# Performance work log

Hardware: AMD Instinct MI355X
Metric: run time of the kernel (lower is better)

Reference implementation:

```python
import jax, jax.numpy as jnp
import numpy as np


def setup_inputs() -> dict:
    key = jax.random.key(0)
    k1, k2, k3, k4 = jax.random.split(key, 4)
    B, S, IN, H = 4, 2048, 512, 1024
    x = jax.random.normal(k1, (B, S, IN), dtype=jnp.float32)
    W1 = jax.random.normal(k2, (IN, H), dtype=jnp.float32) * (1.0 / np.sqrt(IN))
    b1 = jax.random.normal(k3, (H,), dtype=jnp.float32) * 0.02
    Wq = jax.random.normal(k4, (H, H), dtype=jnp.float32) * (1.0 / np.sqrt(H))
    return {"x": x, "W1": W1, "b1": b1, "Wq": Wq, "atten_size": 16}


def reference(x, W1, b1, Wq, atten_size):
    A = atten_size
    B, S, _ = x.shape
    H = W1.shape[1]
    h = jax.nn.relu(jnp.einsum('bsi,ih->bsh', x, W1) + b1)  # [B,S,H]
    # zero-pad sequence dim by A on each side
    padded = jnp.pad(h, ((0, 0), (A, A), (0, 0)))  # [B,S+2A,H]
    # torch: stack(roll(padded, k, 1) for k in -A..A, dim=2) then slice [A:-A]
    # => x_nei[b, i, j] = padded[b, 2A + i - j]
    idx = 2 * A + jnp.arange(S)[:, None] - jnp.arange(2 * A + 1)[None, :]  # [S,W]
    x_nei = padded[:, idx, :]  # [B,S,W,H]
    q = jnp.einsum('bsh,hk->bsk', h, Wq)  # [B,S,H]
    scores = jnp.einsum('bsh,bswh->bsw', q, x_nei) / jnp.sqrt(jnp.asarray(H, x.dtype))
    w = jax.nn.softmax(scores, axis=2)  # softmax over window axis
    out = jnp.einsum('bsw,bswh->bsh', w, x_nei)
    return out
```

## Files before the change

kernel.cpp:

```cpp
#include <hip/hip_runtime.h>
#include <stdint.h>

constexpr int BATCH = 4;
constexpr int SEQ   = 2048;
constexpr int DIN   = 512;
constexpr int DH    = 1024;
constexpr int BS    = BATCH * SEQ;
constexpr int AP    = 32;
constexpr int AW    = 64;

typedef float  floatx4 __attribute__((ext_vector_type(4)));
typedef short  bf16x8  __attribute__((ext_vector_type(8)));

static __device__ __forceinline__ unsigned short f2bf(float f) {
  union { float f; unsigned u; } v; v.f = f;
  unsigned r = (v.u + 0x7fffu + ((v.u >> 16) & 1u)) >> 16;
  return (unsigned short)r;
}

__global__ __launch_bounds__(256) void to_bf16_k(const float* __restrict__ in,
                                                 unsigned short* __restrict__ out, int n) {
  int i = (blockIdx.x * 256 + threadIdx.x) * 4;
  if (i < n) {
    float4 v = *(const float4*)(in + i);
    ushort4 o;
    o.x = f2bf(v.x); o.y = f2bf(v.y); o.z = f2bf(v.z); o.w = f2bf(v.w);
    *(ushort4*)(out + i) = o;
  }
}

__global__ __launch_bounds__(256) void transpose_bf16_k(const float* __restrict__ in,
                                                        unsigned short* __restrict__ out,
                                                        int R, int C) {
  __shared__ float t[32][33];
  int c0 = blockIdx.x * 32, r0 = blockIdx.y * 32;
  int tx = threadIdx.x & 31, ty = threadIdx.x >> 5;
  for (int i = ty; i < 32; i += 8) t[i][tx] = in[(size_t)(r0 + i) * C + c0 + tx];
  __syncthreads();
  for (int i = ty; i < 32; i += 8) out[(size_t)(c0 + i) * R + r0 + tx] = f2bf(t[tx][i]);
}

template <bool RELU>
__global__ __launch_bounds__(256) void gemm_bt(const unsigned short* __restrict__ Ab,
                                               const unsigned short* __restrict__ Bt,
                                               const float* __restrict__ bias,
                                               unsigned short* __restrict__ outB,
                                               unsigned short* __restrict__ outBT,
                                               int M, int N, int K) {
  __shared__ __align__(16) short As[128 * 32];
  __shared__ __align__(16) short Bs[128 * 32];
  const int tid  = threadIdx.x;
  const int m0   = blockIdx.y * 128, n0 = blockIdx.x * 128;
  const int wave = tid >> 6, lane = tid & 63;
  const int wm   = (wave >> 1) * 64, wn = (wave & 1) * 64;
  const int l16  = lane & 15, quad = lane >> 4;

  const int sr = tid >> 1;
  const int sh = (tid & 1) * 16;
  const uint4* gA = (const uint4*)(Ab + (size_t)(m0 + sr) * K + sh);
  const uint4* gB = (const uint4*)(Bt + (size_t)(n0 + sr) * K + sh);
  uint4* lA = (uint4*)&As[sr * 32 + sh];
  uint4* lB = (uint4*)&Bs[sr * 32 + sh];

  floatx4 acc[4][4];
  for (int i = 0; i < 4; i++)
    for (int j = 0; j < 4; j++) acc[i][j] = {0.f, 0.f, 0.f, 0.f};

  const int ksteps = K >> 5;
  for (int ks = 0; ks < ksteps; ++ks) {
    uint4 a0 = gA[0], a1 = gA[1];
    uint4 b0 = gB[0], b1 = gB[1];
    gA += 4; gB += 4;
    __syncthreads();
    lA[0] = a0; lA[1] = a1;
    lB[0] = b0; lB[1] = b1;
    __syncthreads();
    bf16x8 af[4], bfr[4];
    for (int i = 0; i < 4; i++)
      af[i] = *(const bf16x8*)&As[(wm + i * 16 + l16) * 32 + quad * 8];
    for (int j = 0; j < 4; j++)
      bfr[j] = *(const bf16x8*)&Bs[(wn + j * 16 + l16) * 32 + quad * 8];
    for (int i = 0; i < 4; i++)
      for (int j = 0; j < 4; j++)
        acc[i][j] = __builtin_amdgcn_mfma_f32_16x16x32_bf16(af[i], bfr[j], acc[i][j], 0, 0, 0);
  }

  for (int j = 0; j < 4; j++) {
    const int col = n0 + wn + j * 16 + l16;
    const float bv = RELU ? bias[col] : 0.f;
    for (int i = 0; i < 4; i++) {
      const int rowb = m0 + wm + i * 16 + quad * 4;
      float v[4];
      for (int r = 0; r < 4; r++) {
        v[r] = acc[i][j][r] + bv;
        if (RELU) v[r] = fmaxf(v[r], 0.f);
      }
      if (outB) {
        for (int r = 0; r < 4; r++) outB[(size_t)(rowb + r) * N + col] = f2bf(v[r]);
      }
      if (outBT) {
        ushort4 o4; o4.x = f2bf(v[0]); o4.y = f2bf(v[1]); o4.z = f2bf(v[2]); o4.w = f2bf(v[3]);
        *(ushort4*)(outBT + (size_t)col * M + rowb) = o4;
      }
    }
  }
}

__global__ __launch_bounds__(512) void attn_mfma_k(const unsigned short* __restrict__ hb,
                                                   const unsigned short* __restrict__ hbT,
                                                   const unsigned short* __restrict__ qb,
                                                   float* __restrict__ out) {
  __shared__ __align__(16) short Qs[32 * 72];
  __shared__ __align__(16) short Hs[64 * 72];
  __shared__ __align__(16) short Ps[32 * 72];
  __shared__ __align__(16) short Ht[128 * 72];
  __shared__ float Sf[32 * 64];

  const int tid  = threadIdx.x;
  const int wave = tid >> 6, lane = tid & 63;
  const int l16  = lane & 15, quad = lane >> 4;
  const int p0   = blockIdx.x * AP;
  const int s0   = p0 & (SEQ - 1);

  for (int i = tid; i < 32 * 72 / 2; i += 512) ((unsigned*)Ps)[i] = 0;

  const int mtile = wave >> 2;
  const int ntile = wave & 3;
  const bool isQ = tid < 128;
  const bool isH = (tid >= 128) && (tid < 384);
  const int sq = tid & 3;
  int srow = isQ ? (tid >> 2) : ((tid - 128) >> 2);
  bool ldv = false;
  const uint4* gsrc = nullptr;
  short* ldst = nullptr;
  if (isQ) {
    ldv = true;
    gsrc = (const uint4*)(qb + (size_t)(p0 + srow) * DH + sq * 16);
    ldst = &Qs[srow * 72 + sq * 16];
  } else if (isH) {
    const int hj = s0 - 16 + srow;
    ldv = (hj >= 0) && (hj < SEQ);
    gsrc = (const uint4*)(hb + (long long)(p0 - 16 + srow) * DH + sq * 16);
    ldst = &Hs[srow * 72 + sq * 16];
  }

  floatx4 acc = {0.f, 0.f, 0.f, 0.f};
  for (int ks = 0; ks < DH / 64; ++ks) {
    uint4 r0 = {0, 0, 0, 0}, r1 = {0, 0, 0, 0};
    if (ldv) { r0 = gsrc[0]; r1 = gsrc[1]; gsrc += 8; }
    __syncthreads();
    if (isQ || isH) { ((uint4*)ldst)[0] = r0; ((uint4*)ldst)[1] = r1; }
    __syncthreads();
    bf16x8 a0 = *(const bf16x8*)&Qs[(mtile * 16 + l16) * 72 + quad * 8];
    bf16x8 a1 = *(const bf16x8*)&Qs[(mtile * 16 + l16) * 72 + 32 + quad * 8];
    bf16x8 b0 = *(const bf16x8*)&Hs[(ntile * 16 + l16) * 72 + quad * 8];
    bf16x8 b1 = *(const bf16x8*)&Hs[(ntile * 16 + l16) * 72 + 32 + quad * 8];
    acc = __builtin_amdgcn_mfma_f32_16x16x32_bf16(a0, b0, acc, 0, 0, 0);
    acc = __builtin_amdgcn_mfma_f32_16x16x32_bf16(a1, b1, acc, 0, 0, 0);
  }
  for (int r = 0; r < 4; r++)
    Sf[(mtile * 16 + quad * 4 + r) * 64 + ntile * 16 + l16] = acc[r] * (1.f / 32.f);
  __syncthreads();

  {
    const int row = tid >> 4, k = tid & 15;
    const float v0 = Sf[row * 64 + row + k];
    const float v1 = Sf[row * 64 + row + k + 16];
    const float v2 = (k == 0) ? Sf[row * 64 + row + 32] : -1e30f;
    float mx = fmaxf(v0, fmaxf(v1, v2));
    for (int off = 1; off < 16; off <<= 1) mx = fmaxf(mx, __shfl_xor(mx, off, 64));
    const float e0 = __expf(v0 - mx), e1 = __expf(v1 - mx);
    const float e2 = (k == 0) ? __expf(v2 - mx) : 0.f;
    float sum = e0 + e1 + e2;
    for (int off = 1; off < 16; off <<= 1) sum += __shfl_xor(sum, off, 64);
    const float inv = 1.f / sum;
    Ps[row * 72 + row + k] = f2bf(e0 * inv);
    Ps[row * 72 + row + k + 16] = f2bf(e1 * inv);
    if (k == 0) Ps[row * 72 + row + 32] = f2bf(e2 * inv);
  }
  __syncthreads();

  const bf16x8 pa0 = *(const bf16x8*)&Ps[(mtile * 16 + l16) * 72 + quad * 8];
  const bf16x8 pa1 = *(const bf16x8*)&Ps[(mtile * 16 + l16) * 72 + 32 + quad * 8];

  int lo = 16 - s0; if (lo < 0) lo = 0;
  int hi = SEQ + 16 - s0; if (hi > AW) hi = AW;
  const bool interior = (lo == 0) && (hi == AW);
  const int hn = tid >> 2;
  const int ntp = (wave & 3) * 2;

  for (int c = 0; c < DH / 128; ++c) {
    const int nc = c * 128;
    const unsigned short* hp = hbT + ((long long)(nc + hn) * BS + p0 - 16 + sq * 16);
    uint4 r0 = ((const uint4*)hp)[0], r1 = ((const uint4*)hp)[1];
    if (!interior) {
      unsigned short vals[16];
      ((uint4*)vals)[0] = r0; ((uint4*)vals)[1] = r1;
      #pragma unroll
      for (int e = 0; e < 16; e++) {
        const int k = sq * 16 + e;
        if (k < lo || k >= hi) vals[e] = 0;
      }
      r0 = ((uint4*)vals)[0]; r1 = ((uint4*)vals)[1];
    }
    __syncthreads();
    ((uint4*)&Ht[hn * 72 + sq * 16])[0] = r0;
    ((uint4*)&Ht[hn * 72 + sq * 16])[1] = r1;
    __syncthreads();
    floatx4 acc2[2] = {{0.f, 0.f, 0.f, 0.f}, {0.f, 0.f, 0.f, 0.f}};
    for (int t = 0; t < 2; t++) {
      const int nt = ntp + t;
      bf16x8 b0 = *(const bf16x8*)&Ht[(nt * 16 + l16) * 72 + quad * 8];
      bf16x8 b1 = *(const bf16x8*)&Ht[(nt * 16 + l16) * 72 + 32 + quad * 8];
      acc2[t] = __builtin_amdgcn_mfma_f32_16x16x32_bf16(pa0, b0, acc2[t], 0, 0, 0);
      acc2[t] = __builtin_amdgcn_mfma_f32_16x16x32_bf16(pa1, b1, acc2[t], 0, 0, 0);
    }
    for (int t = 0; t < 2; t++) {
      const int col = nc + (ntp + t) * 16 + l16;
      for (int r = 0; r < 4; r++)
        out[(size_t)(p0 + mtile * 16 + quad * 4 + r) * DH + col] = acc2[t][r];
    }
  }
}

extern "C" void kernel_launch(void* const* d_in, const int* in_sizes, int n_in,
                              void* d_out, int out_size, void* d_ws, size_t ws_size,
                              hipStream_t stream) {
  const float* x  = (const float*)d_in[0];
  const float* W1 = (const float*)d_in[1];
  const float* b1 = (const float*)d_in[2];
  const float* Wq = (const float*)d_in[3];

  char* w = (char*)d_ws;
  unsigned short* xb  = (unsigned short*)(w);
  unsigned short* w1t = (unsigned short*)(w + (8ull  << 20));
  unsigned short* wqt = (unsigned short*)(w + (9ull  << 20));
  unsigned short* hb  = (unsigned short*)(w + (11ull << 20));
  unsigned short* hbT = (unsigned short*)(w + (27ull << 20));
  unsigned short* qb  = (unsigned short*)(w + (43ull << 20));

  to_bf16_k<<<(BS * DIN) / (256 * 4), 256, 0, stream>>>(x, xb, BS * DIN);
  transpose_bf16_k<<<dim3(DH / 32, DIN / 32), 256, 0, stream>>>(W1, w1t, DIN, DH);
  transpose_bf16_k<<<dim3(DH / 32, DH / 32), 256, 0, stream>>>(Wq, wqt, DH, DH);

  gemm_bt<true><<<dim3(DH / 128, BS / 128), 256, 0, stream>>>(xb, w1t, b1, hb, hbT, BS, DH, DIN);
  gemm_bt<false><<<dim3(DH / 128, BS / 128), 256, 0, stream>>>(hb, wqt, nullptr, qb, nullptr, BS, DH, DH);

  attn_mfma_k<<<BS / AP, 512, 0, stream>>>(hb, hbT, qb, (float*)d_out);
}
```

Before: 172.2 us.

## Use direct global-to-LDS loads in GEMM and split hT transpose into own kernel

The GEMM tile loads now use global_load_lds to write straight from global memory into shared memory, instead of staging through registers. The LDS layout becomes a per-wave contiguous arrangement. The strided transposed store of h from the first GEMM epilogue moves into a separate tiled transpose kernel that reads the bf16 h back. This aims to cut register pressure and the uncoalesced epilogue writes, at the cost of an extra launch and an extra read and write pass over h.

```diff
diff --git a/kernel.cpp b/kernel.cpp
--- a/kernel.cpp
+++ b/kernel.cpp
@@ -16,6 +16,12 @@
   union { float f; unsigned u; } v; v.f = f;
   unsigned r = (v.u + 0x7fffu + ((v.u >> 16) & 1u)) >> 16;
   return (unsigned short)r;
+}
+
+static __device__ __forceinline__ void gld_lds16(const unsigned short* g, const short* l) {
+  typedef const __attribute__((address_space(1))) void* gvp;
+  typedef __attribute__((address_space(3))) void* lvp;
+  __builtin_amdgcn_global_load_lds((gvp)(uintptr_t)g, (lvp)(unsigned)(uintptr_t)l, 16, 0, 0);
 }
 
 __global__ __launch_bounds__(256) void to_bf16_k(const float* __restrict__ in,
@@ -40,27 +46,50 @@
   for (int i = ty; i < 32; i += 8) out[(size_t)(c0 + i) * R + r0 + tx] = f2bf(t[tx][i]);
 }
 
+__global__ __launch_bounds__(256) void transpose_hb_k(const unsigned short* __restrict__ in,
+                                                      unsigned short* __restrict__ out) {
+  __shared__ __align__(16) unsigned short t[64][80];
+  const int tid = threadIdx.x;
+  const int r0 = blockIdx.x * 64;
+  const int c0 = blockIdx.y * 64;
+  const int tr = tid >> 2, tc = (tid & 3) * 16;
+  const uint4* src = (const uint4*)(in + (size_t)(r0 + tr) * DH + c0 + tc);
+  uint4 v0 = src[0], v1 = src[1];
+  *(uint4*)&t[tr][tc]     = v0;
+  *(uint4*)&t[tr][tc + 8] = v1;
+  __syncthreads();
+  __align__(16) unsigned short vals[16];
+  #pragma unroll
+  for (int e = 0; e < 16; e++) vals[e] = t[tc + e][tr];
+  uint4* dst = (uint4*)(out + (size_t)(c0 + tr) * BS + r0 + tc);
+  dst[0] = ((uint4*)vals)[0];
+  dst[1] = ((uint4*)vals)[1];
+}
+
 template <bool RELU>
 __global__ __launch_bounds__(256) void gemm_bt(const unsigned short* __restrict__ Ab,
                                                const unsigned short* __restrict__ Bt,
                                                const float* __restrict__ bias,
                                                unsigned short* __restrict__ outB,
-                                               unsigned short* __restrict__ outBT,
                                                int M, int N, int K) {
   __shared__ __align__(16) short As[128 * 32];
   __shared__ __align__(16) short Bs[128 * 32];
   const int tid  = threadIdx.x;
   const int m0   = blockIdx.y * 128, n0 = blockIdx.x * 128;
-  const int wave = tid >> 6, lane = tid & 63;
-  const int wm   = (wave >> 1) * 64, wn = (wave & 1) * 64;
+  const int wv   = tid >> 6, lane = tid & 63;
+  const int wm   = (wv >> 1) * 64, wn = (wv & 1) * 64;
   const int l16  = lane & 15, quad = lane >> 4;
 
-  const int sr = tid >> 1;
-  const int sh = (tid & 1) * 16;
-  const uint4* gA = (const uint4*)(Ab + (size_t)(m0 + sr) * K + sh);
-  const uint4* gB = (const uint4*)(Bt + (size_t)(n0 + sr) * K + sh);
-  uint4* lA = (uint4*)&As[sr * 32 + sh];
-  uint4* lB = (uint4*)&Bs[sr * 32 + sh];
+  const int ra = lane >> 2;
+  const int ca = (lane & 3) * 8;
+  const unsigned short* gA0 = Ab + (size_t)(m0 + wv * 32 + ra) * K + ca;
+  const unsigned short* gA1 = Ab + (size_t)(m0 + wv * 32 + 16 + ra) * K + ca;
+  const unsigned short* gB0 = Bt + (size_t)(n0 + wv * 32 + ra) * K + ca;
+  const unsigned short* gB1 = Bt + (size_t)(n0 + wv * 32 + 16 + ra) * K + ca;
+  const short* lA0 = &As[wv * 1024];
+  const short* lA1 = &As[wv * 1024 + 512];
+  const short* lB0 = &Bs[wv * 1024];
+  const short* lB1 = &Bs[wv * 1024 + 512];
 
   floatx4 acc[4][4];
   for (int i = 0; i < 4; i++)
@@ -68,12 +97,10 @@
 
   const int ksteps = K >> 5;
   for (int ks = 0; ks < ksteps; ++ks) {
-    uint4 a0 = gA[0], a1 = gA[1];
-    uint4 b0 = gB[0], b1 = gB[1];
-    gA += 4; gB += 4;
-    __syncthreads();
-    lA[0] = a0; lA[1] = a1;
-    lB[0] = b0; lB[1] = b1;
+    __syncthreads();
+    gld_lds16(gA0, lA0); gld_lds16(gA1, lA1);
+    gld_lds16(gB0, lB0); gld_lds16(gB1, lB1);
+    gA0 += 32; gA1 += 32; gB0 += 32; gB1 += 32;
     __syncthreads();
     bf16x8 af[4], bfr[4];
     for (int i = 0; i < 4; i++)
@@ -90,17 +117,10 @@
     const float bv = RELU ? bias[col] : 0.f;
     for (int i = 0; i < 4; i++) {
       const int rowb = m0 + wm + i * 16 + quad * 4;
-      float v[4];
       for (int r = 0; r < 4; r++) {
-        v[r] = acc[i][j][r] + bv;
-        if (RELU) v[r] = fmaxf(v[r], 0.f);
-      }
-      if (outB) {
-        for (int r = 0; r < 4; r++) outB[(size_t)(rowb + r) * N + col] = f2bf(v[r]);
-      }
-      if (outBT) {
-        ushort4 o4; o4.x = f2bf(v[0]); o4.y = f2bf(v[1]); o4.z = f2bf(v[2]); o4.w = f2bf(v[3]);
-        *(ushort4*)(outBT + (size_t)col * M + rowb) = o4;
+        float v = acc[i][j][r] + bv;
+        if (RELU) v = fmaxf(v, 0.f);
+        outB[(size_t)(rowb + r) * N + col] = f2bf(v);
       }
     }
   }
@@ -243,8 +263,9 @@
   transpose_bf16_k<<<dim3(DH / 32, DIN / 32), 256, 0, stream>>>(W1, w1t, DIN, DH);
   transpose_bf16_k<<<dim3(DH / 32, DH / 32), 256, 0, stream>>>(Wq, wqt, DH, DH);
 
-  gemm_bt<true><<<dim3(DH / 128, BS / 128), 256, 0, stream>>>(xb, w1t, b1, hb, hbT, BS, DH, DIN);
-  gemm_bt<false><<<dim3(DH / 128, BS / 128), 256, 0, stream>>>(hb, wqt, nullptr, qb, nullptr, BS, DH, DH);
+  gemm_bt<true><<<dim3(DH / 128, BS / 128), 256, 0, stream>>>(xb, w1t, b1, hb, BS, DH, DIN);
+  transpose_hb_k<<<dim3(BS / 64, DH / 64), 256, 0, stream>>>(hb, hbT);
+  gemm_bt<false><<<dim3(DH / 128, BS / 128), 256, 0, stream>>>(hb, wqt, nullptr, qb, BS, DH, DH);
 
   attn_mfma_k<<<BS / AP, 512, 0, stream>>>(hb, hbT, qb, (float*)d_out);
 }
```

After: 172.4 us. About the same (+0.1%).
